# Kernel optimization log

Hardware: AMD Instinct MI355X
Metric: run time of the kernel (lower is better)

The kernel has to match this reference:

```python
import jax, jax.numpy as jnp
import numpy as np

N = 4096
INPUT_DIM = 512
H1 = 256
H2 = 64
ALPHA = 0.2
MASK_VAL = -9e15


def setup_inputs() -> dict:
    key = jax.random.key(0)
    ks = jax.random.split(key, 10)

    def glorot(k, fan_in, fan_out):
        r = np.sqrt(6.0 / (fan_in + fan_out)).astype(np.float32)
        return jax.random.uniform(k, (fan_in, fan_out), jnp.float32, -r, r)

    return {
        "X": jax.random.normal(ks[0], (N, INPUT_DIM), jnp.float32),
        "adj": jax.random.randint(ks[1], (N, N), 0, 2, jnp.int32),
        "noise": jax.random.normal(ks[2], (N, H2), jnp.float32),
        "W0": glorot(ks[3], INPUT_DIM, H1),
        "a0": jax.random.normal(ks[4], (2 * H1, 1), jnp.float32) * 0.1,
        "W1": glorot(ks[5], H1, H2),
        "a1": jax.random.normal(ks[6], (2 * H2, 1), jnp.float32) * 0.1,
        "W2": glorot(ks[7], H1, H2),
        "a2": jax.random.normal(ks[8], (2 * H2, 1), jnp.float32) * 0.1,
    }


def gat_layer(X, W, a, adj):
    # h: [N, d]
    h = X @ W
    d = h.shape[1]
    # e_ij = leakyrelu(a^T [h_i ; h_j]) == leakyrelu(f1_i + f2_j)
    f1 = h @ a[:d]            # [N, 1]
    f2 = h @ a[d:]            # [N, 1]
    e = jax.nn.leaky_relu(f1 + f2.T, negative_slope=ALPHA)  # [N, N]
    e = jnp.where(adj > 0, e, MASK_VAL)
    attn = jax.nn.softmax(e, axis=1)  # dropout omitted (eval mode)
    return attn @ h


def reference(X, adj, noise, W0, a0, W1, a1, W2, a2):
    hidden = gat_layer(X, W0, a0, adj)
    mean = gat_layer(hidden, W1, a1, adj)
    logstd = gat_layer(hidden, W2, a2, adj)
    Z = noise * jnp.exp(logstd) + mean          # [N, H2]
    A_pred = jax.nn.sigmoid(Z @ Z.T)            # [N, N]
    return A_pred
```

## Files before the change

### kernel.cpp

```cpp
#include <hip/hip_runtime.h>
#include <hip/hip_bf16.h>
#include <math.h>

#define N_NODES 4096
#define DIM_IN  512
#define DH1     256
#define DH2     64
#define ALPHA   0.2f
#define ROW_WORDS (N_NODES / 64)
#define NWORDS  (N_NODES * ROW_WORDS)
#define L2E     1.4426950408889634f

typedef __bf16 bf16_t;
typedef bf16_t bf16x8 __attribute__((ext_vector_type(8)));
typedef float  f32x4  __attribute__((ext_vector_type(4)));


__global__ __launch_bounds__(256) void prep_kernel(
    const float* __restrict__ X, const float* __restrict__ W0,
    const float* __restrict__ W1, const float* __restrict__ W2,
    const int* __restrict__ adj,
    bf16_t* __restrict__ Xb, bf16_t* __restrict__ W0T,
    bf16_t* __restrict__ W12T, unsigned long long* __restrict__ mask,
    float* __restrict__ f1b, float* __restrict__ f2b)
{
    const int b = blockIdx.x;
    const int tid = threadIdx.x;
    if (b < 2048) {
        int i = b * 256 + tid;
        float4 v = ((const float4*)X)[i];
        bf16_t o[4] = {(bf16_t)v.x, (bf16_t)v.y, (bf16_t)v.z, (bf16_t)v.w};
        const int e = i * 4;
        const int row = e >> 9, k = e & 511;
        const size_t base = ((size_t)(row >> 4) * 64 + (k >> 3)) * 128 + (row & 15) * 8 + (k & 7);
        *(uint2*)(Xb + base) = *(const uint2*)o;
    } else if (b < 2560) {
        int o = (b - 2048) * 256 + tid;
        int n = o >> 9, k = o & 511;
        const size_t base = ((size_t)(n >> 4) * 64 + (k >> 3)) * 128 + (n & 15) * 8 + (k & 7);
        W0T[base] = (bf16_t)W0[(size_t)k * DH1 + n];
    } else if (b < 2688) {
        int o = (b - 2560) * 256 + tid;
        int n = o >> 8, k = o & 255;
        const float* W = (n < 64) ? W1 : W2;
        const size_t base = ((size_t)(n >> 4) * 32 + (k >> 3)) * 128 + (n & 15) * 8 + (k & 7);
        W12T[base] = (bf16_t)W[(size_t)k * 64 + (n & 63)];
    } else if (b < 4736) {
        const int lane = tid & 63;
        int gw = ((b - 2688) * 256 + tid) >> 6;
        for (int w = gw; w < NWORDS; w += 8192) {
            int v = adj[(size_t)w * 64 + lane];
            unsigned long long bb = __ballot(v > 0);
            if (lane == 0) mask[w] = bb;
        }
    } else {
        int zb = b - 4736;
        float4* dst = (float4*)((zb < 8) ? f1b : f2b);
        dst[(zb & 7) * 256 + tid] = float4{0.f, 0.f, 0.f, 0.f};
    }
}

template <int NT, int KLEN>
__global__ __launch_bounds__(256) void attn_fused_kernel(
    const unsigned long long* __restrict__ maskw,
    const float* __restrict__ f1, const float* __restrict__ f2,
    const bf16_t* __restrict__ BT, float* __restrict__ outP,
    float* __restrict__ sOut)
{
    __shared__ float f2s[KLEN];
    __shared__ float tile[64 * (NT * 16 + 4)];
    const int tid = threadIdx.x;
    const int wave = tid >> 6, lane = tid & 63, quad = lane >> 4, l16 = lane & 15;
    const int colBase = blockIdx.x * (NT * 16);
    const int rowBase = blockIdx.y * 64;
    const int kBeg = blockIdx.z * KLEN;
    const int r = rowBase + wave * 16 + l16;

    if (tid < KLEN / 4) ((float4*)f2s)[tid] = *(const float4*)(f2 + kBeg + tid * 4);

    const float f1r = f1[r];

    __syncthreads();

    const int ubase = (colBase >> 4) * (N_NODES * 16) + kBeg * 16;
    const int laneo = quad * 128 + l16 * 8;
    const int qs = quad * 8;
    const unsigned long long* mptr = maskw + (size_t)r * ROW_WORDS + (kBeg >> 6);

    f32x4 acc[NT] = {};
    float ssum = 0.f;
    unsigned long long mcur = mptr[0];
    for (int w = 0; w < KLEN / 64; ++w) {
        unsigned long long mnext = (w < KLEN / 64 - 1) ? mptr[w + 1] : 0ull;
        const unsigned mlo = (unsigned)mcur, mhi = (unsigned)(mcur >> 32);
        #pragma unroll
        for (int h = 0; h < 2; ++h) {
            const int k0 = w * 64 + h * 32;
            bf16x8 bv[NT];
            #pragma unroll
            for (int t = 0; t < NT; ++t)
                bv[t] = *(const bf16x8*)(BT + ubase + t * (N_NODES * 16) + k0 * 16 + laneo);
            const unsigned bits = ((h ? mhi : mlo) >> qs) & 0xFFu;
            const int kc = k0 + qs;
            bf16x8 av;
            #pragma unroll
            for (int j = 0; j < 8; ++j) {
                float x = f1r + f2s[kc + j];
                float e = fmaxf(x, ALPHA * x);
                float p = ((bits >> j) & 1u) ? exp2f(e * L2E) : 0.f;
                ssum += p;
                av[j] = (bf16_t)p;
            }
            #pragma unroll
            for (int t = 0; t < NT; ++t)
                acc[t] = __builtin_amdgcn_mfma_f32_16x16x32_bf16(av, bv[t], acc[t], 0, 0, 0);
        }
        mcur = mnext;
    }

    ssum += __shfl_xor(ssum, 16);
    ssum += __shfl_xor(ssum, 32);
    if (blockIdx.x == 0 && quad == 0)
        sOut[(size_t)blockIdx.z * N_NODES + r] = ssum;

    #pragma unroll
    for (int t = 0; t < NT; ++t) {
        const int col = t * 16 + l16;
        #pragma unroll
        for (int rr = 0; rr < 4; ++rr)
            tile[(wave * 16 + quad * 4 + rr) * (NT * 16 + 4) + col] = acc[t][rr];
    }
    __syncthreads();
    const int half = lane >> 5, c32 = (lane & 31) * 4;
    float* outBase = outP + (size_t)blockIdx.z * N_NODES * DH1 + (size_t)rowBase * DH1 + colBase;
    #pragma unroll
    for (int p = 0; p < 8; ++p) {
        const int rl = p * 8 + wave * 2 + half;
        f32x4 v = *(const f32x4*)&tile[rl * (NT * 16 + 4) + c32];
        __builtin_nontemporal_store(v, (f32x4*)(outBase + (size_t)rl * DH1 + c32));
    }
}

template <int KLEN>
__global__ __launch_bounds__(256) void attn12_kernel(
    const unsigned long long* __restrict__ maskw,
    const float* __restrict__ f1b, const float* __restrict__ f2b,
    const bf16_t* __restrict__ h12T, float* __restrict__ outP,
    float* __restrict__ s12)
{
    __shared__ float f2s[KLEN];
    __shared__ float tile[64 * 68];
    const int l = blockIdx.x;
    const float* f1 = f1b + (size_t)l * N_NODES;
    const float* f2 = f2b + (size_t)l * N_NODES;

    const int tid = threadIdx.x;
    const int wave = tid >> 6, lane = tid & 63, quad = lane >> 4, l16 = lane & 15;
    const int rowBase = blockIdx.y * 64;
    const int kBeg = blockIdx.z * KLEN;
    const int r = rowBase + wave * 16 + l16;

    if (tid < KLEN / 4) ((float4*)f2s)[tid] = *(const float4*)(f2 + kBeg + tid * 4);

    const float f1r = f1[r];

    __syncthreads();

    const int ubase = (l * 4) * (N_NODES * 16) + kBeg * 16;
    const int laneo = quad * 128 + l16 * 8;
    const int qs = quad * 8;
    const unsigned long long* mptr = maskw + (size_t)r * ROW_WORDS + (kBeg >> 6);

    f32x4 acc[4] = {};
    float ssum = 0.f;
    unsigned long long mcur = mptr[0];
    for (int w = 0; w < KLEN / 64; ++w) {
        unsigned long long mnext = (w < KLEN / 64 - 1) ? mptr[w + 1] : 0ull;
        const unsigned mlo = (unsigned)mcur, mhi = (unsigned)(mcur >> 32);
        #pragma unroll
        for (int h = 0; h < 2; ++h) {
            const int k0 = w * 64 + h * 32;
            bf16x8 bv[4];
            #pragma unroll
            for (int t = 0; t < 4; ++t)
                bv[t] = *(const bf16x8*)(h12T + ubase + t * (N_NODES * 16) + k0 * 16 + laneo);
            const unsigned bits = ((h ? mhi : mlo) >> qs) & 0xFFu;
            const int kc = k0 + qs;
            bf16x8 av;
            #pragma unroll
            for (int j = 0; j < 8; ++j) {
                float x = f1r + f2s[kc + j];
                float e = fmaxf(x, ALPHA * x);
                float p = ((bits >> j) & 1u) ? exp2f(e * L2E) : 0.f;
                ssum += p;
                av[j] = (bf16_t)p;
            }
            #pragma unroll
            for (int t = 0; t < 4; ++t)
                acc[t] = __builtin_amdgcn_mfma_f32_16x16x32_bf16(av, bv[t], acc[t], 0, 0, 0);
        }
        mcur = mnext;
    }

    ssum += __shfl_xor(ssum, 16);
    ssum += __shfl_xor(ssum, 32);
    if (quad == 0)
        s12[((size_t)blockIdx.z * 2 + l) * N_NODES + r] = ssum;

    #pragma unroll
    for (int t = 0; t < 4; ++t) {
        const int col = t * 16 + l16;
        #pragma unroll
        for (int rr = 0; rr < 4; ++rr)
            tile[(wave * 16 + quad * 4 + rr) * 68 + col] = acc[t][rr];
    }
    __syncthreads();
    const int q4 = lane >> 4, c16 = (lane & 15) * 4;
    float* outBase = outP + ((size_t)blockIdx.z * 2 + l) * (N_NODES * DH2) + (size_t)rowBase * DH2;
    #pragma unroll
    for (int p = 0; p < 4; ++p) {
        const int rl = p * 16 + wave * 4 + q4;
        f32x4 v = *(const f32x4*)&tile[rl * 68 + c16];
        __builtin_nontemporal_store(v, (f32x4*)(outBase + (size_t)rl * DH2 + c16));
    }
}

__global__ __launch_bounds__(256) void reduce_kernel(
    const float* __restrict__ p, const float* __restrict__ sA, bf16_t* __restrict__ out)
{
    const int n4 = N_NODES * DH1 / 4;
    int i = blockIdx.x * 256 + threadIdx.x;
    const int e = i * 4;
    const int row = e >> 8, k = e & 255;
    float S = sA[row] + sA[N_NODES + row] + sA[2 * N_NODES + row] + sA[3 * N_NODES + row];
    const float inv = (S > 0.f) ? 1.f / S : 0.f;
    float4 a = ((const float4*)p)[i];
    for (int s = 1; s < 4; ++s) {
        float4 b = ((const float4*)p)[(size_t)s * n4 + i];
        a.x += b.x; a.y += b.y; a.z += b.z; a.w += b.w;
    }
    a.x *= inv; a.y *= inv; a.z *= inv; a.w *= inv;
    bf16_t o[4] = {(bf16_t)a.x, (bf16_t)a.y, (bf16_t)a.z, (bf16_t)a.w};
    const size_t base = ((size_t)(row >> 4) * 32 + (k >> 3)) * 128 + (row & 15) * 8 + (k & 7);
    *(uint2*)(out + base) = *(const uint2*)o;
}

__global__ __launch_bounds__(256) void reduce_z_kernel(
    const float* __restrict__ part, const float* __restrict__ s12,
    const float* __restrict__ noise, bf16_t* __restrict__ ZA, bf16_t* __restrict__ ZB)
{
    const int idx = blockIdx.x * 256 + threadIdx.x;
    const int row = idx >> 6;
    const int stride = 2 * N_NODES * DH2;
    float Sm = 0.f, Sl = 0.f, mean = 0.f, ls = 0.f;
    #pragma unroll
    for (int s = 0; s < 4; ++s) {
        Sm   += s12[((size_t)s * 2 + 0) * N_NODES + row];
        Sl   += s12[((size_t)s * 2 + 1) * N_NODES + row];
        mean += part[(size_t)s * stride + idx];
        ls   += part[(size_t)s * stride + N_NODES * DH2 + idx];
    }
    mean *= (Sm > 0.f) ? 1.f / Sm : 0.f;
    ls   *= (Sl > 0.f) ? 1.f / Sl : 0.f;
    float z = noise[idx] * __expf(ls) + mean;
    bf16_t zhi = (bf16_t)z;
    bf16_t zlo = (bf16_t)(z - (float)zhi);
    const int i = idx >> 6, c = idx & 63;
    const size_t base = ((size_t)(i >> 4) * 32 + (c >> 3)) * 128 + (i & 15) * 8 + (c & 7);
    ZA[base]        = zhi;
    ZA[base + 1024] = zhi;
    ZA[base + 2048] = zlo;
    ZA[base + 3072] = zlo;
    ZB[base]        = zhi;
    ZB[base + 1024] = zlo;
    ZB[base + 2048] = zhi;
    ZB[base + 3072] = zlo;
}

template <int NT>
__global__ __launch_bounds__(256) void gemm0_kernel(
    const bf16_t* __restrict__ A, const bf16_t* __restrict__ BT,
    bf16_t* __restrict__ Ct, const float* __restrict__ a0,
    float* __restrict__ f1, float* __restrict__ f2)
{
    const int tid = threadIdx.x;
    const int wave = tid >> 6, lane = tid & 63, quad = lane >> 4, l16 = lane & 15;
    const int colBase = blockIdx.x * (NT * 16), rowBase = blockIdx.y * 64;
    const size_t KS = (size_t)DIM_IN * 16;
    const bf16_t* Ap = A + (size_t)((rowBase >> 4) + wave) * KS + quad * 128 + l16 * 8;
    const bf16_t* Bp = BT + (size_t)(colBase >> 4) * KS + quad * 128 + l16 * 8;

    f32x4 acc[NT] = {};
    for (int k0 = 0; k0 < DIM_IN; k0 += 64) {
        bf16x8 bv[2 * NT];
        #pragma unroll
        for (int t = 0; t < NT; ++t) {
            bv[t]      = *(const bf16x8*)(Bp + (size_t)t * KS + k0 * 16);
            bv[NT + t] = *(const bf16x8*)(Bp + (size_t)t * KS + (k0 + 32) * 16);
        }
        bf16x8 av0 = *(const bf16x8*)(Ap + k0 * 16);
        bf16x8 av1 = *(const bf16x8*)(Ap + (k0 + 32) * 16);
        #pragma unroll
        for (int t = 0; t < NT; ++t)
            acc[t] = __builtin_amdgcn_mfma_f32_16x16x32_bf16(av0, bv[t], acc[t], 0, 0, 0);
        #pragma unroll
        for (int t = 0; t < NT; ++t)
            acc[t] = __builtin_amdgcn_mfma_f32_16x16x32_bf16(av1, bv[NT + t], acc[t], 0, 0, 0);
    }
    #pragma unroll
    for (int t = 0; t < NT; ++t) {
        const int col = colBase + t * 16 + l16;
        bf16_t pk[4];
        #pragma unroll
        for (int rr = 0; rr < 4; ++rr) pk[rr] = (bf16_t)acc[t][rr];
        const int kc = (rowBase + wave * 16 + quad * 4) >> 3;
        const size_t o = ((size_t)(col >> 4) * (N_NODES >> 3) + kc) * 128
                       + (col & 15) * 8 + (quad & 1) * 4;
        *(uint2*)(Ct + o) = *(const uint2*)pk;
    }
    #pragma unroll
    for (int rr = 0; rr < 4; ++rr) {
        float s1 = 0.f, s2 = 0.f;
        #pragma unroll
        for (int t = 0; t < NT; ++t) {
            const int col = colBase + t * 16 + l16;
            s1 += acc[t][rr] * a0[col];
            s2 += acc[t][rr] * a0[DH1 + col];
        }
        #pragma unroll
        for (int off = 8; off; off >>= 1) {
            s1 += __shfl_down(s1, off, 16);
            s2 += __shfl_down(s2, off, 16);
        }
        if (l16 == 0) {
            const int row = rowBase + wave * 16 + quad * 4 + rr;
            atomicAdd(f1 + row, s1);
            atomicAdd(f2 + row, s2);
        }
    }
}

__global__ __launch_bounds__(256) void gemm12_kernel(
    const bf16_t* __restrict__ A, const bf16_t* __restrict__ BT,
    bf16_t* __restrict__ Ct, const float* __restrict__ a1, const float* __restrict__ a2,
    float* __restrict__ f1b, float* __restrict__ f2b)
{
    const int tid = threadIdx.x;
    const int wave = tid >> 6, lane = tid & 63, quad = lane >> 4, l16 = lane & 15;
    const int l = blockIdx.x;
    const int colBase = l * 64, rowBase = blockIdx.y * 64;
    const size_t KS = (size_t)DH1 * 16;
    const bf16_t* Ap = A + (size_t)((rowBase >> 4) + wave) * KS + quad * 128 + l16 * 8;
    const bf16_t* Bp = BT + (size_t)(colBase >> 4) * KS + quad * 128 + l16 * 8;

    f32x4 acc[4] = {};
    for (int k0 = 0; k0 < DH1; k0 += 64) {
        bf16x8 bv[8];
        #pragma unroll
        for (int t = 0; t < 4; ++t) {
            bv[t]     = *(const bf16x8*)(Bp + (size_t)t * KS + k0 * 16);
            bv[4 + t] = *(const bf16x8*)(Bp + (size_t)t * KS + (k0 + 32) * 16);
        }
        bf16x8 av0 = *(const bf16x8*)(Ap + k0 * 16);
        bf16x8 av1 = *(const bf16x8*)(Ap + (k0 + 32) * 16);
        #pragma unroll
        for (int t = 0; t < 4; ++t)
            acc[t] = __builtin_amdgcn_mfma_f32_16x16x32_bf16(av0, bv[t], acc[t], 0, 0, 0);
        #pragma unroll
        for (int t = 0; t < 4; ++t)
            acc[t] = __builtin_amdgcn_mfma_f32_16x16x32_bf16(av1, bv[4 + t], acc[t], 0, 0, 0);
    }
    #pragma unroll
    for (int t = 0; t < 4; ++t) {
        const int col = colBase + t * 16 + l16;
        bf16_t pk[4];
        #pragma unroll
        for (int rr = 0; rr < 4; ++rr) pk[rr] = (bf16_t)acc[t][rr];
        const int kc = (rowBase + wave * 16 + quad * 4) >> 3;
        const size_t o = ((size_t)(col >> 4) * (N_NODES >> 3) + kc) * 128
                       + (col & 15) * 8 + (quad & 1) * 4;
        *(uint2*)(Ct + o) = *(const uint2*)pk;
    }
    const float* a = l ? a2 : a1;
    #pragma unroll
    for (int rr = 0; rr < 4; ++rr) {
        float s1 = 0.f, s2 = 0.f;
        #pragma unroll
        for (int t = 0; t < 4; ++t) {
            const int lc = t * 16 + l16;
            s1 += acc[t][rr] * a[lc];
            s2 += acc[t][rr] * a[64 + lc];
        }
        #pragma unroll
        for (int off = 8; off; off >>= 1) {
            s1 += __shfl_down(s1, off, 16);
            s2 += __shfl_down(s2, off, 16);
        }
        if (l16 == 0) {
            const int row = rowBase + wave * 16 + quad * 4 + rr;
            f1b[l * N_NODES + row] = s1;
            f2b[l * N_NODES + row] = s2;
        }
    }
}

template <int NT>
__global__ __launch_bounds__(256) void zzt_sigmoid_kernel(
    const bf16_t* __restrict__ ZA, const bf16_t* __restrict__ ZB, float* __restrict__ C)
{
    __shared__ float tile[64 * (NT * 16 + 4)];
    const int tid = threadIdx.x;
    const int wave = tid >> 6, lane = tid & 63, quad = lane >> 4, l16 = lane & 15;
    const int colBase = blockIdx.x * (NT * 16), rowBase = blockIdx.y * 64;
    const bf16_t* Ap = ZA + (size_t)((rowBase >> 4) + wave) * 4096 + quad * 128 + l16 * 8;
    const bf16_t* Bp = ZB + (size_t)(colBase >> 4) * 4096 + quad * 128 + l16 * 8;

    f32x4 acc[NT] = {};
    for (int k0 = 0; k0 < 256; k0 += 32) {
        bf16x8 bv[NT];
        #pragma unroll
        for (int t = 0; t < NT; ++t)
            bv[t] = *(const bf16x8*)(Bp + (size_t)t * 4096 + k0 * 16);
        bf16x8 av = *(const bf16x8*)(Ap + k0 * 16);
        #pragma unroll
        for (int t = 0; t < NT; ++t)
            acc[t] = __builtin_amdgcn_mfma_f32_16x16x32_bf16(av, bv[t], acc[t], 0, 0, 0);
    }
    #pragma unroll
    for (int t = 0; t < NT; ++t) {
        const int col = t * 16 + l16;
        #pragma unroll
        for (int rr = 0; rr < 4; ++rr) {
            const int rl = wave * 16 + quad * 4 + rr;
            float x = acc[t][rr];
            tile[rl * (NT * 16 + 4) + col] = __builtin_amdgcn_rcpf(1.0f + exp2f(-x * L2E));
        }
    }
    __syncthreads();
    const int half = lane >> 5, c32 = (lane & 31) * 4;
    float* outBase = C + (size_t)rowBase * N_NODES + colBase;
    #pragma unroll
    for (int p = 0; p < 8; ++p) {
        const int rl = p * 8 + wave * 2 + half;
        f32x4 v = *(const f32x4*)&tile[rl * (NT * 16 + 4) + c32];
        __builtin_nontemporal_store(v, (f32x4*)(outBase + (size_t)rl * N_NODES + c32));
    }
}

extern "C" void kernel_launch(void* const* d_in, const int* in_sizes, int n_in,
                              void* d_out, int out_size, void* d_ws, size_t ws_size,
                              hipStream_t stream)
{
    const float* X     = (const float*)d_in[0];
    const int*   adj   = (const int*)  d_in[1];
    const float* noise = (const float*)d_in[2];
    const float* W0    = (const float*)d_in[3];
    const float* a0    = (const float*)d_in[4];
    const float* W1    = (const float*)d_in[5];
    const float* a1    = (const float*)d_in[6];
    const float* W2    = (const float*)d_in[7];
    const float* a2    = (const float*)d_in[8];
    float* out = (float*)d_out;

    char* ws = (char*)d_ws;
    size_t off = 0;
    auto alloc = [&](size_t bytes) { char* p = ws + off; off += (bytes + 255) & ~(size_t)255; return p; };

    unsigned long long* mask = (unsigned long long*)alloc((size_t)NWORDS * 8);
    float*  part  = (float*)alloc((size_t)4 * N_NODES * DH1 * 4);
    bf16_t* Xb    = (bf16_t*)alloc((size_t)N_NODES * DIM_IN * 2);
    bf16_t* W0T   = (bf16_t*)alloc((size_t)DH1 * DIM_IN * 2);
    bf16_t* W12T  = (bf16_t*)alloc((size_t)128 * DH1 * 2);
    bf16_t* h0T   = (bf16_t*)alloc((size_t)DH1 * N_NODES * 2);
    bf16_t* hidb  = (bf16_t*)alloc((size_t)N_NODES * DH1 * 2);
    bf16_t* h12T  = (bf16_t*)alloc((size_t)128 * N_NODES * 2);
    bf16_t* ZA    = (bf16_t*)alloc((size_t)N_NODES * 256 * 2);
    bf16_t* ZB    = (bf16_t*)alloc((size_t)N_NODES * 256 * 2);
    float* f1b  = (float*)alloc((size_t)2 * N_NODES * 4);
    float* f2b  = (float*)alloc((size_t)2 * N_NODES * 4);
    float* sA   = (float*)alloc((size_t)4 * N_NODES * 4);
    float* s12  = (float*)alloc((size_t)4 * 2 * N_NODES * 4);
    (void)ws_size; (void)in_sizes; (void)n_in; (void)out_size;

    dim3 blk(256);

    prep_kernel<<<4752, blk, 0, stream>>>(X, W0, W1, W2, adj, Xb, W0T, W12T, mask, f1b, f2b);

    gemm0_kernel<2><<<dim3(8, N_NODES / 64), blk, 0, stream>>>(
        Xb, W0T, h0T, a0, f1b, f2b);
    attn_fused_kernel<8, 1024><<<dim3(2, N_NODES / 64, 4), blk, 0, stream>>>(
        mask, f1b, f2b, h0T, part, sA);
    reduce_kernel<<<1024, blk, 0, stream>>>(part, sA, hidb);

    gemm12_kernel<<<dim3(2, N_NODES / 64), blk, 0, stream>>>(
        hidb, W12T, h12T, a1, a2, f1b, f2b);

    attn12_kernel<1024><<<dim3(2, N_NODES / 64, 4), blk, 0, stream>>>(
        mask, f1b, f2b, h12T, part, s12);
    reduce_z_kernel<<<1024, blk, 0, stream>>>(part, s12, noise, ZA, ZB);

    zzt_sigmoid_kernel<8><<<dim3(N_NODES / 128, N_NODES / 64), blk, 0, stream>>>(
        ZA, ZB, out);
}
```

Before: 232.2 us.

## Exploit symmetry of Z·Zᵀ by computing only upper-triangular tiles and mirroring

The final sigmoid(Z Zᵀ) kernel now launches a 1D triangular grid of tiles, decoding each block id into a (column, row) tile pair. Off-diagonal tiles also write their transpose from shared memory to the mirrored location, which roughly halves the MFMA work. The output write volume is unchanged, and the mirrored writes read the LDS tile column-wise with a padded stride of 133 floats. The kernel is likely bound by output stores, so the gain may be limited, and the triangular index decode adds some per-block work.

```diff
diff --git a/kernel.cpp b/kernel.cpp
--- a/kernel.cpp
+++ b/kernel.cpp
@@ -408,10 +408,18 @@
 __global__ __launch_bounds__(256) void zzt_sigmoid_kernel(
     const bf16_t* __restrict__ ZA, const bf16_t* __restrict__ ZB, float* __restrict__ C)
 {
-    __shared__ float tile[64 * (NT * 16 + 4)];
+    __shared__ float tile[64 * 133];
     const int tid = threadIdx.x;
     const int wave = tid >> 6, lane = tid & 63, quad = lane >> 4, l16 = lane & 15;
-    const int colBase = blockIdx.x * (NT * 16), rowBase = blockIdx.y * 64;
+
+    const int bid = blockIdx.x;
+    int bx = (int)((sqrtf((float)(4 * bid + 1)) - 1.f) * 0.5f);
+    while ((bx + 1) * (bx + 2) <= bid) ++bx;
+    while (bx * (bx + 1) > bid) --bx;
+    const int by = bid - bx * (bx + 1);
+    const bool mirror = (by < 2 * bx);
+    const int colBase = bx * (NT * 16), rowBase = by * 64;
+
     const bf16_t* Ap = ZA + (size_t)((rowBase >> 4) + wave) * 4096 + quad * 128 + l16 * 8;
     const bf16_t* Bp = ZB + (size_t)(colBase >> 4) * 4096 + quad * 128 + l16 * 8;
 
@@ -433,7 +441,7 @@
         for (int rr = 0; rr < 4; ++rr) {
             const int rl = wave * 16 + quad * 4 + rr;
             float x = acc[t][rr];
-            tile[rl * (NT * 16 + 4) + col] = __builtin_amdgcn_rcpf(1.0f + exp2f(-x * L2E));
+            tile[rl * 133 + col] = __builtin_amdgcn_rcpf(1.0f + exp2f(-x * L2E));
         }
     }
     __syncthreads();
@@ -442,8 +450,21 @@
     #pragma unroll
     for (int p = 0; p < 8; ++p) {
         const int rl = p * 8 + wave * 2 + half;
-        f32x4 v = *(const f32x4*)&tile[rl * (NT * 16 + 4) + c32];
+        f32x4 v = *(const f32x4*)&tile[rl * 133 + c32];
         __builtin_nontemporal_store(v, (f32x4*)(outBase + (size_t)rl * N_NODES + c32));
+    }
+    if (mirror) {
+        const int cq = lane >> 4;
+        const int r4 = (lane & 15) * 4;
+        float* mBase = C + (size_t)colBase * N_NODES + rowBase;
+        #pragma unroll
+        for (int p = 0; p < 8; ++p) {
+            const int c = p * 16 + wave * 4 + cq;
+            f32x4 v;
+            #pragma unroll
+            for (int i = 0; i < 4; ++i) v[i] = tile[(r4 + i) * 133 + c];
+            __builtin_nontemporal_store(v, (f32x4*)(mBase + (size_t)c * N_NODES + r4));
+        }
     }
 }
 
@@ -499,6 +520,5 @@
         mask, f1b, f2b, h12T, part, s12);
     reduce_z_kernel<<<1024, blk, 0, stream>>>(part, s12, noise, ZA, ZB);
 
-    zzt_sigmoid_kernel<8><<<dim3(N_NODES / 128, N_NODES / 64), blk, 0, stream>>>(
-        ZA, ZB, out);
-}
+    zzt_sigmoid_kernel<8><<<dim3(1056), blk, 0, stream>>>(ZA, ZB, out);
+}
```

Result: no change. 229.5 us (-1.1%).
